# Kernel tuning notes

Measured on AMD Instinct MI355X. Metric: run time of the kernel, lower is better.

Reference implementation:

```python
import jax, jax.numpy as jnp
import numpy as np
import math

N_HEADS = 16
D_MODEL = 1024
HEAD_DIM = D_MODEL // N_HEADS
ROPE_THETA = 10000.0


def _rope_cos_sin(seq_len, head_dim, dtype):
    # freqs = 1/theta^(2i/d), angles = outer(t, freqs)  -> [seq_len, head_dim//2]
    inv_freq = 1.0 / (ROPE_THETA ** (jnp.arange(0, head_dim, 2, dtype=jnp.float32) / head_dim))
    ang = jnp.arange(seq_len, dtype=jnp.float32)[:, None] * inv_freq[None, :]
    return jnp.cos(ang).astype(dtype), jnp.sin(ang).astype(dtype)


def _apply_rope(t, cos, sin):
    # t: [B, N, H, D]; treat last dim as complex pairs (a, b); multiply by e^{i*ang}
    B, N, H, D = t.shape
    tr = t.reshape(B, N, H, D // 2, 2)
    a, b = tr[..., 0], tr[..., 1]
    c = cos[None, :, None, :]  # [1, N, 1, D/2]
    s = sin[None, :, None, :]
    out = jnp.stack([a * c - b * s, a * s + b * c], axis=-1)
    return out.reshape(B, N, H, D)


def setup_inputs() -> dict:
    key = jax.random.key(0)
    ks = jax.random.split(key, 9)
    B, N, D = 4, 2048, D_MODEL
    scale = 0.02
    inp = {"x": jax.random.normal(ks[0], (B, N, D), dtype=jnp.float32)}
    for i, nm in enumerate(["q", "k", "v", "o"]):
        inp[f"w{nm}"] = jax.random.normal(ks[1 + 2 * i], (D, D), dtype=jnp.float32) * scale
        inp[f"b{nm}"] = jax.random.normal(ks[2 + 2 * i], (D,), dtype=jnp.float32) * scale
    return inp


def reference(x, wq, bq, wk, bk, wv, bv, wo, bo):
    B, N, D = x.shape
    H, Hd = N_HEADS, HEAD_DIM
    q = (x @ wq.T + bq).reshape(B, N, H, Hd)
    k = (x @ wk.T + bk).reshape(B, N, H, Hd)
    v = (x @ wv.T + bv).reshape(B, N, H, Hd)
    cos, sin = _rope_cos_sin(N, Hd, x.dtype)
    q = _apply_rope(q, cos, sin)
    k = _apply_rope(k, cos, sin)
    # SDPA, no mask, eval mode (dropout_p = 0)
    scores = jnp.einsum("bqhd,bkhd->bhqk", q, k) / math.sqrt(Hd)
    attn = jax.nn.softmax(scores, axis=-1)
    out = jnp.einsum("bhqk,bkhd->bqhd", attn, v)  # [B, N, H, Hd]
    out = out.reshape(B, N, D)
    return out @ wo.T + bo
```

## Files before the change

### kernel.cpp

```cpp
#include <hip/hip_runtime.h>
#include <math.h>
#include <stdint.h>

#define BBATCH 4
#define NTOK   2048
#define DMOD   1024
#define NH     16
#define HD     64
#define MTOT   8192

typedef __bf16 bf16;
typedef __bf16 bf16x2 __attribute__((ext_vector_type(2)));
typedef __bf16 bf16x4 __attribute__((ext_vector_type(4)));
typedef __bf16 bf16x8 __attribute__((ext_vector_type(8)));
typedef float  f32x4  __attribute__((ext_vector_type(4)));
typedef float  f32x16 __attribute__((ext_vector_type(16)));
typedef unsigned int u32;
typedef unsigned int u32x2 __attribute__((ext_vector_type(2)));
typedef unsigned int u32x4 __attribute__((ext_vector_type(4)));

typedef __attribute__((address_space(3))) unsigned int lds_u32;
typedef __attribute__((address_space(1))) unsigned int glb_u32;

__device__ __forceinline__ void gload16(const bf16* g, bf16* l) {
    __builtin_amdgcn_global_load_lds((glb_u32*)g, (lds_u32*)l, 16, 0, 0);
}

__device__ __forceinline__ u32 pack_bf16(float lo, float hi) {
    bf16x2 z; z[0] = (bf16)lo; z[1] = (bf16)hi;
    return __builtin_bit_cast(u32, z);
}

#define MFMA32(a, b, c) __builtin_amdgcn_mfma_f32_32x32x16_bf16((a), (b), (c), 0, 0, 0)

#define QSCALE 0.1803368801111204f

__global__ void rope_table_kernel(float* __restrict__ ct, float* __restrict__ st) {
    int idx = blockIdx.x * 256 + threadIdx.x;
    if (idx >= NTOK * 32) return;
    int n = idx >> 5, p = idx & 31;
    float inv = powf(10000.0f, -(float)(2 * p) / 64.0f);
    float ang = (float)n * inv;
    ct[idx] = cosf(ang);
    st[idx] = sinf(ang);
}

__global__ __launch_bounds__(256)
void convert_kernel(const float* __restrict__ x,  const float* __restrict__ wq,
                    const float* __restrict__ wk, const float* __restrict__ wv,
                    const float* __restrict__ wo,
                    bf16* __restrict__ xb,  bf16* __restrict__ wqb,
                    bf16* __restrict__ wkb, bf16* __restrict__ wvb,
                    bf16* __restrict__ wob)
{
    const int X4 = (MTOT * DMOD) / 4;
    const int W4 = (DMOD * DMOD) / 4;
    int i = blockIdx.x * 256 + threadIdx.x;
    const float* src; bf16* dst; int off;
    if (i < X4) { src = x; dst = xb; off = i; }
    else {
        int j = i - X4; int w = j / W4; off = j - w * W4;
        src = (w == 0) ? wq : (w == 1) ? wk : (w == 2) ? wv : wo;
        dst = (w == 0) ? wqb : (w == 1) ? wkb : (w == 2) ? wvb : wob;
    }
    float4 v = ((const float4*)src)[off];
    bf16x4 o;
    o[0] = (bf16)v.x; o[1] = (bf16)v.y; o[2] = (bf16)v.z; o[3] = (bf16)v.w;
    *(bf16x4*)(dst + (size_t)off * 4) = o;
}


#define GEMM_PROLOGUE(Aptr, Wptr)                                              \
    __shared__ __align__(16) bf16 As[2][128 * 32];                             \
    __shared__ __align__(16) bf16 Bs[2][128 * 32];                             \
    const int tid = threadIdx.x;                                               \
    const int l   = tid & 63;                                                  \
    const int wid = tid >> 6;                                                  \
    const int wm  = wid >> 1, wn = wid & 1;                                    \
    const int fr  = l & 15, fg = l >> 4;                                       \
    const int srow  = tid >> 2;                                                \
    const int sslot = (tid & 3) ^ ((srow >> 1) & 3);                           \
    const bf16* gA0 = (Aptr) + (size_t)(m0 + srow) * 1024 + sslot * 8;         \
    const bf16* gB0 = (Wptr) + (size_t)(n0 + srow) * 1024 + sslot * 8;         \
    const int aswz = (fg ^ ((fr >> 1) & 3)) * 8;                               \
    int aoff[4], boff[4];                                                      \
    _Pragma("unroll")                                                          \
    for (int i = 0; i < 4; ++i) {                                              \
        aoff[i] = (wm * 64 + i * 16 + fr) * 32 + aswz;                         \
        boff[i] = (wn * 64 + i * 16 + fr) * 32 + aswz;                         \
    }                                                                          \
    f32x4 acc[4][4] = {};

#define GSTAGE(kt, b) do {                                         \
        const bf16* a0_ = gA0 + (kt) * 32;                         \
        const bf16* b0_ = gB0 + (kt) * 32;                         \
        gload16(a0_,                      As[b] + tid * 8);        \
        gload16(a0_ + (size_t)64 * 1024,  As[b] + 2048 + tid * 8); \
        gload16(b0_,                      Bs[b] + tid * 8);        \
        gload16(b0_ + (size_t)64 * 1024,  Bs[b] + 2048 + tid * 8); \
    } while (0)

#define GEMM_KLOOP                                                             \
    GSTAGE(0, 0);                                                              \
    __syncthreads();                                                           \
    int cur = 0;                                                               \
    for (int kt = 0; kt < 32; ++kt) {                                          \
        if (kt < 31) GSTAGE(kt + 1, cur ^ 1);                                  \
        bf16x8 af[4], bfv[4];                                                  \
        _Pragma("unroll")                                                      \
        for (int i = 0; i < 4; ++i) af[i]  = *(const bf16x8*)(As[cur] + aoff[i]); \
        _Pragma("unroll")                                                      \
        for (int i = 0; i < 4; ++i) bfv[i] = *(const bf16x8*)(Bs[cur] + boff[i]); \
        _Pragma("unroll")                                                      \
        for (int mi = 0; mi < 4; ++mi)                                         \
            _Pragma("unroll")                                                  \
            for (int ni = 0; ni < 4; ++ni)                                     \
                acc[mi][ni] = __builtin_amdgcn_mfma_f32_16x16x32_bf16(         \
                    af[mi], bfv[ni], acc[mi][ni], 0, 0, 0);                    \
        __syncthreads();                                                       \
        cur ^= 1;                                                              \
    }

__global__ __launch_bounds__(256)
void gemm_qkv(const bf16* __restrict__ A,
              const bf16* __restrict__ wq, const bf16* __restrict__ wk,
              const bf16* __restrict__ wv,
              const float* __restrict__ bq, const float* __restrict__ bk,
              const float* __restrict__ bv,
              bf16* __restrict__ qb, bf16* __restrict__ kb, bf16* __restrict__ vtb,
              const float* __restrict__ ct, const float* __restrict__ st)
{
    const int sel = blockIdx.x >> 3;
    const int n0  = (blockIdx.x & 7) * 128;
    const int m0  = blockIdx.y * 128;
    const bf16*  W    = (sel == 0) ? wq : (sel == 1) ? wk : wv;
    const float* bias = (sel == 0) ? bq : (sel == 1) ? bk : bv;
    bf16*        out  = (sel == 0) ? qb : (sel == 1) ? kb : vtb;

    GEMM_PROLOGUE(A, W)
    GEMM_KLOOP

    if (sel == 2) {
#pragma unroll
        for (int ni = 0; ni < 4; ++ni) {
            const int col = n0 + wn * 64 + ni * 16 + fr;
            const int h = col >> 6, dd = col & 63;
            const float bvv = bias[col];
#pragma unroll
            for (int mi = 0; mi < 4; ++mi) {
                const int rowb = m0 + wm * 64 + mi * 16 + fg * 4;
                const int bi = rowb >> 11, npb = rowb & (NTOK - 1);
                bf16x4 ov;
#pragma unroll
                for (int r = 0; r < 4; ++r) ov[r] = (bf16)(acc[mi][ni][r] + bvv);
                *(bf16x4*)(out + ((size_t)(bi * NH + h) * HD + dd) * NTOK + npb) = ov;
            }
        }
    } else {
        const float scale = (sel == 0) ? QSCALE : 1.0f;
#pragma unroll
        for (int ni = 0; ni < 4; ++ni) {
            const int col = n0 + wn * 64 + ni * 16 + fr;
            const int h = col >> 6, dd = col & 63, p = (dd >> 1);
            const float bvv = bias[col];
#pragma unroll
            for (int mi = 0; mi < 4; ++mi) {
                const int rowb = m0 + wm * 64 + mi * 16 + fg * 4;
#pragma unroll
                for (int r = 0; r < 4; ++r) {
                    const int row = rowb + r;
                    const int bi = row >> 11, np = row & (NTOK - 1);
                    float v  = acc[mi][ni][r] + bvv;
                    float pv = __shfl_xor(v, 1);
                    float c = ct[np * 32 + p], s = st[np * 32 + p];
                    float o = (dd & 1) ? (pv * s + v * c) : (v * c - pv * s);
                    o *= scale;
                    out[((size_t)(bi * NH + h) * NTOK + np) * HD + dd] = (bf16)o;
                }
            }
        }
    }
}

__global__ __launch_bounds__(256)
void gemm_oproj(const bf16* __restrict__ A, const bf16* __restrict__ W,
                const float* __restrict__ bias, float* __restrict__ out)
{
    const int m0 = blockIdx.y * 128, n0 = blockIdx.x * 128;
    GEMM_PROLOGUE(A, W)
    GEMM_KLOOP
#pragma unroll
    for (int ni = 0; ni < 4; ++ni) {
        const int col = n0 + wn * 64 + ni * 16 + fr;
        const float bv = bias[col];
#pragma unroll
        for (int mi = 0; mi < 4; ++mi) {
            const int rowb = m0 + wm * 64 + mi * 16 + fg * 4;
#pragma unroll
            for (int r = 0; r < 4; ++r)
                out[(size_t)(rowb + r) * 1024 + col] = acc[mi][ni][r] + bv;
        }
    }
}

__global__ __launch_bounds__(256)
void attn_mfma(const bf16* __restrict__ Q, const bf16* __restrict__ K,
               const bf16* __restrict__ Vt, bf16* __restrict__ out)
{
    __shared__ __align__(16) bf16 Ks[2][64 * 64];
    __shared__ __align__(16) bf16 Vs[2][64 * 64];

    const int tid = threadIdx.x;
    const int l   = tid & 63;
    const int wid = tid >> 6;
    const int lq  = l & 31;
    const int hi  = l >> 5;
    const int rx  = lq & 7;
    const int q0 = blockIdx.x * 128;
    const int bh = blockIdx.y;

    const bf16* Qb = Q  + (size_t)bh * NTOK * HD;
    const bf16* Kb = K  + (size_t)bh * NTOK * HD;
    const bf16* Vb = Vt + (size_t)bh * HD * NTOK;

    bf16x8 qf[4];
#pragma unroll
    for (int c = 0; c < 4; ++c)
        qf[c] = *(const bf16x8*)(Qb + (size_t)(q0 + wid * 32 + lq) * HD + c * 16 + hi * 8);

    bf16x8 ones;
#pragma unroll
    for (int i = 0; i < 8; ++i) ones[i] = (bf16)1.0f;

    const int srow  = tid >> 3;
    const int sslot = (tid & 7) ^ (srow & 7);
    const bf16* gK0 = Kb + (size_t)srow * HD + sslot * 8;
    const bf16* gV0 = Vb + (size_t)srow * NTOK + sslot * 8;

#define ASTAGE(t, b) do {                                          \
        const bf16* gK_ = gK0 + (size_t)(t) * 64 * HD;             \
        const bf16* gV_ = gV0 + (size_t)(t) * 64;                  \
        gload16(gK_,                      Ks[b] + tid * 8);        \
        gload16(gK_ + 32 * HD,            Ks[b] + 2048 + tid * 8); \
        gload16(gV_,                      Vs[b] + tid * 8);        \
        gload16(gV_ + (size_t)32 * NTOK,  Vs[b] + 2048 + tid * 8); \
    } while (0)

    f32x16 o0 = {}, o1 = {};
    f32x16 l4 = {};

    ASTAGE(0, 0);
    __syncthreads();
    int cur = 0;

    for (int t = 0; t < 32; ++t) {
        if (t < 31) ASTAGE(t + 1, cur ^ 1);
        const bf16* Kc = Ks[cur];
        const bf16* Vc = Vs[cur];

        f32x16 t0 = {}, t1 = {};
#pragma unroll
        for (int c = 0; c < 4; ++c) {
            const int slot = ((c * 2 + hi) ^ rx) * 8;
            bf16x8 kf0 = *(const bf16x8*)(Kc + lq * 64 + slot);
            bf16x8 kf1 = *(const bf16x8*)(Kc + (32 + lq) * 64 + slot);
            t0 = MFMA32(kf0, qf[c], t0);
            t1 = MFMA32(kf1, qf[c], t1);
        }

#pragma unroll
        for (int r = 0; r < 16; ++r) t0[r] = __builtin_amdgcn_exp2f(t0[r]);
#pragma unroll
        for (int r = 0; r < 16; ++r) t1[r] = __builtin_amdgcn_exp2f(t1[r]);

#pragma unroll
        for (int b = 0; b < 2; ++b) {
            const f32x16& tb = b ? t1 : t0;
#pragma unroll
            for (int kc = 0; kc < 2; ++kc) {
                const int a0 = kc ? 8 : 0;
                const int a1 = kc ? 12 : 4;
                u32 X  = pack_bf16(tb[a0],     tb[a0 + 1]);
                u32 Y  = pack_bf16(tb[a1],     tb[a1 + 1]);
                u32 X2 = pack_bf16(tb[a0 + 2], tb[a0 + 3]);
                u32 Y2 = pack_bf16(tb[a1 + 2], tb[a1 + 3]);
                u32x2 s0 = __builtin_amdgcn_permlane32_swap(X,  Y,  false, false);
                u32x2 s1 = __builtin_amdgcn_permlane32_swap(X2, Y2, false, false);
                u32x4 bw;
                bw[0] = s0[0]; bw[1] = s1[0]; bw[2] = s0[1]; bw[3] = s1[1];
                const bf16x8 pf = __builtin_bit_cast(bf16x8, bw);

                const int slot = (((b * 4 + kc * 2) + hi) ^ rx) * 8;
                bf16x8 vf0 = *(const bf16x8*)(Vc + lq * 64 + slot);
                bf16x8 vf1 = *(const bf16x8*)(Vc + (32 + lq) * 64 + slot);
                o0 = MFMA32(vf0, pf, o0);
                o1 = MFMA32(vf1, pf, o1);
                l4 = MFMA32(ones, pf, l4);
            }
        }

        __syncthreads();
        cur ^= 1;
    }
#undef ASTAGE

    const int b_ = bh >> 4, h = bh & 15;
    const float inv = 1.0f / l4[0];
    const int token = q0 + wid * 32 + lq;
    bf16* dst = out + (size_t)(b_ * NTOK + token) * DMOD + h * HD;
#pragma unroll
    for (int dblk = 0; dblk < 2; ++dblk) {
        const f32x16& ob = dblk ? o1 : o0;
#pragma unroll
        for (int g = 0; g < 4; ++g) {
            bf16x4 ov;
#pragma unroll
            for (int r2 = 0; r2 < 4; ++r2) ov[r2] = (bf16)(ob[g * 4 + r2] * inv);
            *(bf16x4*)(dst + dblk * 32 + g * 8 + hi * 4) = ov;
        }
    }
}

extern "C" void kernel_launch(void* const* d_in, const int* in_sizes, int n_in,
                              void* d_out, int out_size, void* d_ws, size_t ws_size,
                              hipStream_t stream)
{
    (void)in_sizes; (void)n_in; (void)out_size; (void)ws_size;

    const float* x  = (const float*)d_in[0];
    const float* wq = (const float*)d_in[1];
    const float* bq = (const float*)d_in[2];
    const float* wk = (const float*)d_in[3];
    const float* bk = (const float*)d_in[4];
    const float* wv = (const float*)d_in[5];
    const float* bv = (const float*)d_in[6];
    const float* wo = (const float*)d_in[7];
    const float* bo = (const float*)d_in[8];
    float* out = (float*)d_out;

    const size_t XSZ = (size_t)MTOT * DMOD;
    const size_t WSZ = (size_t)DMOD * DMOD;
    bf16* xb  = (bf16*)d_ws;
    bf16* wqb = xb  + XSZ;
    bf16* wkb = wqb + WSZ;
    bf16* wvb = wkb + WSZ;
    bf16* wob = wvb + WSZ;
    bf16* qb  = wob + WSZ;
    bf16* kb  = qb  + XSZ;
    bf16* vtb = kb  + XSZ;
    bf16* ab  = vtb + XSZ;
    float* ct = (float*)(ab + XSZ);
    float* st = ct + (size_t)NTOK * 32;

    rope_table_kernel<<<dim3(256), dim3(256), 0, stream>>>(ct, st);
    convert_kernel<<<dim3(12288), dim3(256), 0, stream>>>(x, wq, wk, wv, wo,
                                                          xb, wqb, wkb, wvb, wob);

    gemm_qkv<<<dim3(24, MTOT / 128), dim3(256), 0, stream>>>(
        xb, wqb, wkb, wvb, bq, bk, bv, qb, kb, vtb, ct, st);

    attn_mfma<<<dim3(NTOK / 128, BBATCH * NH), dim3(256), 0, stream>>>(qb, kb, vtb, ab);

    gemm_oproj<<<dim3(DMOD / 128, MTOT / 128), dim3(256), 0, stream>>>(ab, wob, bo, out);
}
```

Before: 325.9 us.

## Enlarge QKV GEMM tile to 256x128 and fold RoPE table into convert

The QKV projection GEMM now uses 512-thread blocks computing 256x128 output tiles. The 128-row weight tile in shared memory is shared by eight waves instead of four, which roughly halves weight reloads from global memory. The RoPE cos/sin table generation moves into the first 256 blocks of the conversion kernel, removing one kernel launch. The trade-offs are more shared memory per block, half as many QKV blocks (768), and possibly lower occupancy; the O-projection GEMM is just inlined with unchanged behaviour.

```diff
diff --git a/kernel.cpp b/kernel.cpp
--- a/kernel.cpp
+++ b/kernel.cpp
@@ -35,24 +35,24 @@
 
 #define QSCALE 0.1803368801111204f
 
-__global__ void rope_table_kernel(float* __restrict__ ct, float* __restrict__ st) {
-    int idx = blockIdx.x * 256 + threadIdx.x;
-    if (idx >= NTOK * 32) return;
-    int n = idx >> 5, p = idx & 31;
-    float inv = powf(10000.0f, -(float)(2 * p) / 64.0f);
-    float ang = (float)n * inv;
-    ct[idx] = cosf(ang);
-    st[idx] = sinf(ang);
-}
-
 __global__ __launch_bounds__(256)
 void convert_kernel(const float* __restrict__ x,  const float* __restrict__ wq,
                     const float* __restrict__ wk, const float* __restrict__ wv,
                     const float* __restrict__ wo,
                     bf16* __restrict__ xb,  bf16* __restrict__ wqb,
                     bf16* __restrict__ wkb, bf16* __restrict__ wvb,
-                    bf16* __restrict__ wob)
+                    bf16* __restrict__ wob,
+                    float* __restrict__ ct, float* __restrict__ st)
 {
+    if (blockIdx.x < 256) {
+        int idx = blockIdx.x * 256 + threadIdx.x;
+        int n = idx >> 5, p = idx & 31;
+        float inv = powf(10000.0f, -(float)(2 * p) / 64.0f);
+        float ang = (float)n * inv;
+        ct[idx] = cosf(ang);
+        st[idx] = sinf(ang);
+    }
+
     const int X4 = (MTOT * DMOD) / 4;
     const int W4 = (DMOD * DMOD) / 4;
     int i = blockIdx.x * 256 + threadIdx.x;
@@ -69,59 +69,7 @@
     *(bf16x4*)(dst + (size_t)off * 4) = o;
 }
 
-
-#define GEMM_PROLOGUE(Aptr, Wptr)                                              \
-    __shared__ __align__(16) bf16 As[2][128 * 32];                             \
-    __shared__ __align__(16) bf16 Bs[2][128 * 32];                             \
-    const int tid = threadIdx.x;                                               \
-    const int l   = tid & 63;                                                  \
-    const int wid = tid >> 6;                                                  \
-    const int wm  = wid >> 1, wn = wid & 1;                                    \
-    const int fr  = l & 15, fg = l >> 4;                                       \
-    const int srow  = tid >> 2;                                                \
-    const int sslot = (tid & 3) ^ ((srow >> 1) & 3);                           \
-    const bf16* gA0 = (Aptr) + (size_t)(m0 + srow) * 1024 + sslot * 8;         \
-    const bf16* gB0 = (Wptr) + (size_t)(n0 + srow) * 1024 + sslot * 8;         \
-    const int aswz = (fg ^ ((fr >> 1) & 3)) * 8;                               \
-    int aoff[4], boff[4];                                                      \
-    _Pragma("unroll")                                                          \
-    for (int i = 0; i < 4; ++i) {                                              \
-        aoff[i] = (wm * 64 + i * 16 + fr) * 32 + aswz;                         \
-        boff[i] = (wn * 64 + i * 16 + fr) * 32 + aswz;                         \
-    }                                                                          \
-    f32x4 acc[4][4] = {};
-
-#define GSTAGE(kt, b) do {                                         \
-        const bf16* a0_ = gA0 + (kt) * 32;                         \
-        const bf16* b0_ = gB0 + (kt) * 32;                         \
-        gload16(a0_,                      As[b] + tid * 8);        \
-        gload16(a0_ + (size_t)64 * 1024,  As[b] + 2048 + tid * 8); \
-        gload16(b0_,                      Bs[b] + tid * 8);        \
-        gload16(b0_ + (size_t)64 * 1024,  Bs[b] + 2048 + tid * 8); \
-    } while (0)
-
-#define GEMM_KLOOP                                                             \
-    GSTAGE(0, 0);                                                              \
-    __syncthreads();                                                           \
-    int cur = 0;                                                               \
-    for (int kt = 0; kt < 32; ++kt) {                                          \
-        if (kt < 31) GSTAGE(kt + 1, cur ^ 1);                                  \
-        bf16x8 af[4], bfv[4];                                                  \
-        _Pragma("unroll")                                                      \
-        for (int i = 0; i < 4; ++i) af[i]  = *(const bf16x8*)(As[cur] + aoff[i]); \
-        _Pragma("unroll")                                                      \
-        for (int i = 0; i < 4; ++i) bfv[i] = *(const bf16x8*)(Bs[cur] + boff[i]); \
-        _Pragma("unroll")                                                      \
-        for (int mi = 0; mi < 4; ++mi)                                         \
-            _Pragma("unroll")                                                  \
-            for (int ni = 0; ni < 4; ++ni)                                     \
-                acc[mi][ni] = __builtin_amdgcn_mfma_f32_16x16x32_bf16(         \
-                    af[mi], bfv[ni], acc[mi][ni], 0, 0, 0);                    \
-        __syncthreads();                                                       \
-        cur ^= 1;                                                              \
-    }
-
-__global__ __launch_bounds__(256)
+__global__ __launch_bounds__(512)
 void gemm_qkv(const bf16* __restrict__ A,
               const bf16* __restrict__ wq, const bf16* __restrict__ wk,
               const bf16* __restrict__ wv,
@@ -130,15 +78,68 @@
               bf16* __restrict__ qb, bf16* __restrict__ kb, bf16* __restrict__ vtb,
               const float* __restrict__ ct, const float* __restrict__ st)
 {
+    __shared__ __align__(16) bf16 As[2][256 * 32];
+    __shared__ __align__(16) bf16 Bs[2][128 * 32];
+
     const int sel = blockIdx.x >> 3;
     const int n0  = (blockIdx.x & 7) * 128;
-    const int m0  = blockIdx.y * 128;
+    const int m0  = blockIdx.y * 256;
     const bf16*  W    = (sel == 0) ? wq : (sel == 1) ? wk : wv;
     const float* bias = (sel == 0) ? bq : (sel == 1) ? bk : bv;
     bf16*        out  = (sel == 0) ? qb : (sel == 1) ? kb : vtb;
 
-    GEMM_PROLOGUE(A, W)
-    GEMM_KLOOP
+    const int tid = threadIdx.x;
+    const int l   = tid & 63;
+    const int wid = tid >> 6;
+    const int wm  = wid >> 1, wn = wid & 1;
+    const int fr  = l & 15, fg = l >> 4;
+
+    const int srow  = tid >> 2;
+    const int sslot = (tid & 3) ^ ((srow >> 1) & 3);
+    const bf16* gA0 = A + (size_t)(m0 + srow) * 1024 + sslot * 8;
+    const bf16* gB0 = W + (size_t)(n0 + srow) * 1024 + sslot * 8;
+
+    const int aswz = (fg ^ ((fr >> 1) & 3)) * 8;
+    int aoff[4], boff[4];
+#pragma unroll
+    for (int i = 0; i < 4; ++i) {
+        aoff[i] = (wm * 64 + i * 16 + fr) * 32 + aswz;
+        boff[i] = (wn * 64 + i * 16 + fr) * 32 + aswz;
+    }
+
+    f32x4 acc[4][4] = {};
+
+#define QSTAGE(kt, b) do {                                           \
+        const bf16* a0_ = gA0 + (kt) * 32;                           \
+        const bf16* b0_ = gB0 + (kt) * 32;                           \
+        gload16(a0_,                       As[b] + tid * 8);         \
+        gload16(a0_ + (size_t)128 * 1024,  As[b] + 4096 + tid * 8);  \
+        gload16(b0_,                       Bs[b] + tid * 8);         \
+    } while (0)
+
+    QSTAGE(0, 0);
+    __syncthreads();
+    int cur = 0;
+
+    for (int kt = 0; kt < 32; ++kt) {
+        if (kt < 31) QSTAGE(kt + 1, cur ^ 1);
+
+        bf16x8 af[4], bfv[4];
+#pragma unroll
+        for (int i = 0; i < 4; ++i) af[i]  = *(const bf16x8*)(As[cur] + aoff[i]);
+#pragma unroll
+        for (int i = 0; i < 4; ++i) bfv[i] = *(const bf16x8*)(Bs[cur] + boff[i]);
+#pragma unroll
+        for (int mi = 0; mi < 4; ++mi)
+#pragma unroll
+            for (int ni = 0; ni < 4; ++ni)
+                acc[mi][ni] = __builtin_amdgcn_mfma_f32_16x16x32_bf16(
+                    af[mi], bfv[ni], acc[mi][ni], 0, 0, 0);
+
+        __syncthreads();
+        cur ^= 1;
+    }
+#undef QSTAGE
 
     if (sel == 2) {
 #pragma unroll
@@ -186,9 +187,64 @@
 void gemm_oproj(const bf16* __restrict__ A, const bf16* __restrict__ W,
                 const float* __restrict__ bias, float* __restrict__ out)
 {
+    __shared__ __align__(16) bf16 As[2][128 * 32];
+    __shared__ __align__(16) bf16 Bs[2][128 * 32];
+
     const int m0 = blockIdx.y * 128, n0 = blockIdx.x * 128;
-    GEMM_PROLOGUE(A, W)
-    GEMM_KLOOP
+    const int tid = threadIdx.x;
+    const int l   = tid & 63;
+    const int wid = tid >> 6;
+    const int wm  = wid >> 1, wn = wid & 1;
+    const int fr  = l & 15, fg = l >> 4;
+
+    const int srow  = tid >> 2;
+    const int sslot = (tid & 3) ^ ((srow >> 1) & 3);
+    const bf16* gA0 = A + (size_t)(m0 + srow) * 1024 + sslot * 8;
+    const bf16* gB0 = W + (size_t)(n0 + srow) * 1024 + sslot * 8;
+
+    const int aswz = (fg ^ ((fr >> 1) & 3)) * 8;
+    int aoff[4], boff[4];
+#pragma unroll
+    for (int i = 0; i < 4; ++i) {
+        aoff[i] = (wm * 64 + i * 16 + fr) * 32 + aswz;
+        boff[i] = (wn * 64 + i * 16 + fr) * 32 + aswz;
+    }
+
+    f32x4 acc[4][4] = {};
+
+#define OSTAGE(kt, b) do {                                          \
+        const bf16* a0_ = gA0 + (kt) * 32;                          \
+        const bf16* b0_ = gB0 + (kt) * 32;                          \
+        gload16(a0_,                      As[b] + tid * 8);         \
+        gload16(a0_ + (size_t)64 * 1024,  As[b] + 2048 + tid * 8);  \
+        gload16(b0_,                      Bs[b] + tid * 8);         \
+        gload16(b0_ + (size_t)64 * 1024,  Bs[b] + 2048 + tid * 8);  \
+    } while (0)
+
+    OSTAGE(0, 0);
+    __syncthreads();
+    int cur = 0;
+
+    for (int kt = 0; kt < 32; ++kt) {
+        if (kt < 31) OSTAGE(kt + 1, cur ^ 1);
+
+        bf16x8 af[4], bfv[4];
+#pragma unroll
+        for (int i = 0; i < 4; ++i) af[i]  = *(const bf16x8*)(As[cur] + aoff[i]);
+#pragma unroll
+        for (int i = 0; i < 4; ++i) bfv[i] = *(const bf16x8*)(Bs[cur] + boff[i]);
+#pragma unroll
+        for (int mi = 0; mi < 4; ++mi)
+#pragma unroll
+            for (int ni = 0; ni < 4; ++ni)
+                acc[mi][ni] = __builtin_amdgcn_mfma_f32_16x16x32_bf16(
+                    af[mi], bfv[ni], acc[mi][ni], 0, 0, 0);
+
+        __syncthreads();
+        cur ^= 1;
+    }
+#undef OSTAGE
+
 #pragma unroll
     for (int ni = 0; ni < 4; ++ni) {
         const int col = n0 + wn * 64 + ni * 16 + fr;
@@ -352,11 +408,11 @@
     float* ct = (float*)(ab + XSZ);
     float* st = ct + (size_t)NTOK * 32;
 
-    rope_table_kernel<<<dim3(256), dim3(256), 0, stream>>>(ct, st);
     convert_kernel<<<dim3(12288), dim3(256), 0, stream>>>(x, wq, wk, wv, wo,
-                                                          xb, wqb, wkb, wvb, wob);
-
-    gemm_qkv<<<dim3(24, MTOT / 128), dim3(256), 0, stream>>>(
+                                                          xb, wqb, wkb, wvb, wob,
+                                                          ct, st);
+
+    gemm_qkv<<<dim3(24, MTOT / 256), dim3(512), 0, stream>>>(
         xb, wqb, wkb, wvb, bq, bk, bv, qb, kb, vtb, ct, st);
 
     attn_mfma<<<dim3(NTOK / 128, BBATCH * NH), dim3(256), 0, stream>>>(qb, kb, vtb, ab);
```

Measured after the change: 321.4 us. About the same (-1.4%).
